# Kernel tuning notes

Hardware: AMD Instinct MI355X
Metric: run time of the kernel (lower is better)

The kernel has to match this reference:

```python
import jax, jax.numpy as jnp
import numpy as np

OUT, IN, GS = 16384, 4096, 16
G = OUT * IN // GS  # 4194304 groups


def setup_inputs() -> dict:
    key = jax.random.key(0)
    k1, k2, k3, k4 = jax.random.split(key, 4)
    x = jax.random.normal(k1, (8, 32, IN), dtype=jnp.float32)
    weight_q2 = jax.random.randint(k2, (G, GS // 4), 0, 256, dtype=jnp.int32)
    weight_norm = jax.random.uniform(k3, (G, 1), dtype=jnp.float16)
    bias = jax.random.normal(k4, (OUT,), dtype=jnp.float32)
    return {"x": x, "weight_q2": weight_q2, "weight_norm": weight_norm, "bias": bias}


def _dequant_2bit(weight_q2, weight_norm):
    # torch: xq_out[:, i::4] = (xq >> 2i) & 3  =>  element index within group = i + 4*k
    # where k = packed column (slow, stride 4), i = shift index (fast).
    norm = weight_norm.astype(jnp.float32)                      # [G, 1]
    shifts = jnp.arange(4, dtype=jnp.int32) * 2                 # [4]
    vals = (weight_q2[:, :, None] >> shifts) & 3                # [G, 4(pack k), 4(shift i)]
    xq_out = vals.astype(jnp.float32).reshape(G, GS)            # [G, 16], layout k*4 + i
    w = (xq_out / 3.0) * (2.0 * norm) - norm                    # [G, 16]
    return w.reshape(OUT, IN)


def reference(x, weight_q2, weight_norm, bias):
    w = _dequant_2bit(weight_q2, weight_norm)                   # [OUT, IN] fp32
    return jnp.einsum('bsi,oi->bso', x, w) + bias
```

## Files before the change

### kernel.cpp

```cpp
#include <hip/hip_runtime.h>
#include <stdint.h>

#define M_DIM 256
#define N_DIM 16384
#define K_DIM 4096
#define BN 32
#define BM 128
#define BK 128
#define NT2 (K_DIM / BK)

typedef __bf16 bf16x8 __attribute__((ext_vector_type(8)));
typedef float  f32x4  __attribute__((ext_vector_type(4)));

__device__ __forceinline__ uint32_t f2bf(float f) {
  uint32_t u = __float_as_uint(f);
  return (u + 0x7fffu + ((u >> 16) & 1u)) >> 16;
}

#define LDS_BARRIER() \
  asm volatile("s_waitcnt lgkmcnt(0)\n\ts_barrier" ::: "memory")

__global__ __launch_bounds__(256) void cvt_x_kernel(const float* __restrict__ x,
                                                    uint4* __restrict__ ws) {
  int T = blockIdx.x * 256 + threadIdx.x;
  int mb_glob = T >> 13;
  int r       = T & 8191;
  int kch     = r >> 6;
  int L       = r & 63;
  int row = mb_glob * 16 + (L & 15);
  int k   = kch * 32 + (L >> 4) * 8;
  const float* p = x + (size_t)row * K_DIM + k;
  float4 a = *(const float4*)p;
  float4 b = *(const float4*)(p + 4);
  uint4 o;
  o.x = f2bf(a.x) | (f2bf(a.y) << 16);
  o.y = f2bf(a.z) | (f2bf(a.w) << 16);
  o.z = f2bf(b.x) | (f2bf(b.y) << 16);
  o.w = f2bf(b.z) | (f2bf(b.w) << 16);
  ws[T] = o;
}

__device__ __forceinline__ uint4 deq8(uint2 q, float nv) {
  float a2 = nv * (2.0f / 3.0f);
  uint32_t tlo = f2bf(-nv) | (f2bf(fmaf(1.0f, a2, -nv)) << 16);
  uint32_t thi = f2bf(fmaf(2.0f, a2, -nv)) | (f2bf(fmaf(3.0f, a2, -nv)) << 16);
  uint32_t s0 = ((q.x & 3u) | ((q.x & 0xCu) << 14)) * 0x0202u + 0x01000100u;
  uint32_t s1 = (((q.x >> 4) & 3u) | ((q.x & 0xC0u) << 10)) * 0x0202u + 0x01000100u;
  uint32_t s2 = ((q.y & 3u) | ((q.y & 0xCu) << 14)) * 0x0202u + 0x01000100u;
  uint32_t s3 = (((q.y >> 4) & 3u) | ((q.y & 0xC0u) << 10)) * 0x0202u + 0x01000100u;
  uint4 r;
  r.x = __builtin_amdgcn_perm(thi, tlo, s0);
  r.y = __builtin_amdgcn_perm(thi, tlo, s1);
  r.z = __builtin_amdgcn_perm(thi, tlo, s2);
  r.w = __builtin_amdgcn_perm(thi, tlo, s3);
  return r;
}

__global__ __launch_bounds__(256, 4) void gemm2bit_kernel(
    const uint4*    __restrict__ aws,
    const uint32_t* __restrict__ q2,
    const float*    __restrict__ nrm,
    const float*    __restrict__ bias,
    float*          __restrict__ out)
{
  __shared__ uint4 Bb[2][512];

  const int tid  = threadIdx.x;
  const int lane = tid & 63;
  const int w    = tid >> 6;
  const int lo4  = lane & 15;
  const int qd   = lane >> 4;
  const int n0   = blockIdx.x * BN;
  const int m0   = blockIdx.y * BM;

  const int lrs = lane ^ qd;

  const int nloc = tid >> 3;
  const int kg   = (tid >> 1) & 3;
  const int h    = tid & 1;
  const int grow = n0 + nloc;
  const int qd2  = (kg & 1) * 2 + h;
  const int swz  = (nloc & 15) ^ qd2;
  const int bs0 = ((kg >> 1) * 2 + (nloc >> 4)) * 64 + qd2 * 16 + swz;
  const int bs1 = ((2 + (kg >> 1)) * 2 + (nloc >> 4)) * 64 + qd2 * 16 + swz;

  const uint4* pA = aws + (size_t)(blockIdx.y * 8 + w * 2) * 8192 + lane;
  const uint32_t* pq = q2 + ((size_t)grow * 256 + kg) * 4 + h * 2;
  const float*    pn = nrm + (size_t)grow * 256 + kg;

  f32x4 acc[2][2];
#pragma unroll
  for (int s = 0; s < 2; ++s)
#pragma unroll
    for (int u = 0; u < 2; ++u)
      acc[s][u] = (f32x4){0.f, 0.f, 0.f, 0.f};

  uint4 af0[8], af1[8];
  uint2 qa0, qa1, qb0, qb1;
  float na0, na1, nb0, nb1;

#pragma unroll
  for (int s = 0; s < 2; ++s)
#pragma unroll
    for (int c = 0; c < 4; ++c)
      af0[s * 4 + c] = pA[s * 8192 + c * 64];
  {
    uint2 x0 = *(const uint2*)pq;
    uint2 x1 = *(const uint2*)(pq + 16);
    float y0 = pn[0], y1 = pn[4];
    qa0 = *(const uint2*)(pq + 32);  qa1 = *(const uint2*)(pq + 48);
    na0 = pn[8];  na1 = pn[12];
    qb0 = *(const uint2*)(pq + 64);  qb1 = *(const uint2*)(pq + 80);
    nb0 = pn[16]; nb1 = pn[20];
    Bb[0][bs0] = deq8(x0, y0);
    Bb[0][bs1] = deq8(x1, y1);
  }
  LDS_BARRIER();
  const uint4* pAp = pA + 256;

#define GEMM_BODY(T, PR, AFC, AFN, Q0, Q1, N0v, N1v)                            \
  do {                                                                          \
    if ((T) + 1 < NT2) {                                                        \
      _Pragma("unroll")                                                         \
      for (int s = 0; s < 2; ++s)                                               \
        _Pragma("unroll")                                                       \
        for (int c = 0; c < 4; ++c)                                             \
          AFN[s * 4 + c] = pAp[s * 8192 + c * 64];                              \
    }                                                                           \
    _Pragma("unroll")                                                           \
    for (int c = 0; c < 4; ++c) {                                               \
      bf16x8 bfv[2];                                                            \
      _Pragma("unroll")                                                         \
      for (int u = 0; u < 2; ++u)                                               \
        bfv[u] = *(const bf16x8*)&Bb[PR][(c * 2 + u) * 64 + lrs];               \
      _Pragma("unroll")                                                         \
      for (int s = 0; s < 2; ++s) {                                             \
        bf16x8 av = __builtin_bit_cast(bf16x8, AFC[s * 4 + c]);                 \
        _Pragma("unroll")                                                       \
        for (int u = 0; u < 2; ++u)                                             \
          acc[s][u] = __builtin_amdgcn_mfma_f32_16x16x32_bf16(av, bfv[u],       \
                                                              acc[s][u], 0, 0, 0);\
      }                                                                         \
    }                                                                           \
    if ((T) + 1 < NT2) {                                                        \
      Bb[(PR) ^ 1][bs0] = deq8(Q0, N0v);                                        \
      Bb[(PR) ^ 1][bs1] = deq8(Q1, N1v);                                        \
    }                                                                           \
    if ((T) + 3 < NT2) {                                                        \
      Q0  = *(const uint2*)(pq + (size_t)((T) + 3) * 32);                       \
      Q1  = *(const uint2*)(pq + (size_t)((T) + 3) * 32 + 16);                  \
      N0v = pn[(size_t)((T) + 3) * 8];                                          \
      N1v = pn[(size_t)((T) + 3) * 8 + 4];                                      \
    }                                                                           \
    pAp += 256;                                                                 \
    LDS_BARRIER();                                                              \
  } while (0)

  for (int t2 = 0; t2 < NT2; t2 += 2) {
    GEMM_BODY(t2,     0, af0, af1, qa0, qa1, na0, na1);
    GEMM_BODY(t2 + 1, 1, af1, af0, qb0, qb1, nb0, nb1);
  }
#undef GEMM_BODY

  float bv[2];
#pragma unroll
  for (int u = 0; u < 2; ++u)
    bv[u] = bias[n0 + u * 16 + lo4];

#pragma unroll
  for (int s = 0; s < 2; ++s) {
    int mrow = m0 + w * 32 + s * 16 + qd * 4;
#pragma unroll
    for (int u = 0; u < 2; ++u) {
      int ncol = n0 + u * 16 + lo4;
      float* p = out + (size_t)mrow * N_DIM + ncol;
#pragma unroll
      for (int r = 0; r < 4; ++r)
        p[(size_t)r * N_DIM] = acc[s][u][r] + bv[u];
    }
  }
}

extern "C" void kernel_launch(void* const* d_in, const int* in_sizes, int n_in,
                              void* d_out, int out_size, void* d_ws, size_t ws_size,
                              hipStream_t stream) {
  const float*    x    = (const float*)d_in[0];
  const uint32_t* q2   = (const uint32_t*)d_in[1];
  const float*    nm   = (const float*)d_in[2];
  const float*    bias = (const float*)d_in[3];
  float*          out  = (float*)d_out;
  uint4*          aws  = (uint4*)d_ws;

  cvt_x_kernel<<<512, 256, 0, stream>>>(x, aws);
  gemm2bit_kernel<<<dim3(N_DIM / BN, 2), 256, 0, stream>>>(aws, q2, nm, bias, out);
}
```

Baseline: 176.1 us.

## Widen N tile to 64 with 512-thread blocks and 2x4 warp grid

Doubles the per-block N tile to 64 columns and uses 8 waves arranged as 4 (M) by 2 (N), so each block dequantizes 64 weight rows into a larger LDS buffer and each A fragment load serves twice the N columns. The dequant store is split between two halves of the MFMA loop, and s_setprio is raised around the MFMA sections so matrix work interleaves with the dequant and load work. The aim is to halve redundant loads of the converted activations per weight tile and improve latency hiding. In exchange, the grid has half as many blocks, each block is larger, and register and LDS pressure per block go up.

```diff
diff --git a/kernel.cpp b/kernel.cpp
--- a/kernel.cpp
+++ b/kernel.cpp
@@ -4,8 +4,7 @@
 #define M_DIM 256
 #define N_DIM 16384
 #define K_DIM 4096
-#define BN 32
-#define BM 128
+#define BN 64
 #define BK 128
 #define NT2 (K_DIM / BK)
 
@@ -56,22 +55,24 @@
   return r;
 }
 
-__global__ __launch_bounds__(256, 4) void gemm2bit_kernel(
+__global__ __launch_bounds__(512, 4) void gemm2bit_kernel(
     const uint4*    __restrict__ aws,
     const uint32_t* __restrict__ q2,
     const float*    __restrict__ nrm,
     const float*    __restrict__ bias,
     float*          __restrict__ out)
 {
-  __shared__ uint4 Bb[2][512];
+  __shared__ uint4 Bb[2][1024];
 
   const int tid  = threadIdx.x;
   const int lane = tid & 63;
   const int w    = tid >> 6;
+  const int wm   = w >> 1;
+  const int wn   = w & 1;
   const int lo4  = lane & 15;
   const int qd   = lane >> 4;
   const int n0   = blockIdx.x * BN;
-  const int m0   = blockIdx.y * BM;
+  const int m0   = blockIdx.y * 128;
 
   const int lrs = lane ^ qd;
 
@@ -80,11 +81,10 @@
   const int h    = tid & 1;
   const int grow = n0 + nloc;
   const int qd2  = (kg & 1) * 2 + h;
-  const int swz  = (nloc & 15) ^ qd2;
-  const int bs0 = ((kg >> 1) * 2 + (nloc >> 4)) * 64 + qd2 * 16 + swz;
-  const int bs1 = ((2 + (kg >> 1)) * 2 + (nloc >> 4)) * 64 + qd2 * 16 + swz;
-
-  const uint4* pA = aws + (size_t)(blockIdx.y * 8 + w * 2) * 8192 + lane;
+  const int bs1 = ((kg >> 1) * 4 + (nloc >> 4)) * 64 + qd2 * 16 +
+                  ((nloc & 15) ^ qd2);
+
+  const uint4* pA = aws + (size_t)(blockIdx.y * 8 + wm * 2) * 8192 + lane;
   const uint32_t* pq = q2 + ((size_t)grow * 256 + kg) * 4 + h * 2;
   const float*    pn = nrm + (size_t)grow * 256 + kg;
 
@@ -96,83 +96,95 @@
       acc[s][u] = (f32x4){0.f, 0.f, 0.f, 0.f};
 
   uint4 af0[8], af1[8];
-  uint2 qa0, qa1, qb0, qb1;
-  float na0, na1, nb0, nb1;
+  uint2 qE1, qE2, qO1, qO2;
+  float nE1, nE2, nO1, nO2;
 
 #pragma unroll
   for (int s = 0; s < 2; ++s)
 #pragma unroll
     for (int c = 0; c < 4; ++c)
-      af0[s * 4 + c] = pA[s * 8192 + c * 64];
+      af0[s * 4 + c] = pA[(size_t)s * 8192 + c * 64];
   {
-    uint2 x0 = *(const uint2*)pq;
-    uint2 x1 = *(const uint2*)(pq + 16);
-    float y0 = pn[0], y1 = pn[4];
-    qa0 = *(const uint2*)(pq + 32);  qa1 = *(const uint2*)(pq + 48);
-    na0 = pn[8];  na1 = pn[12];
-    qb0 = *(const uint2*)(pq + 64);  qb1 = *(const uint2*)(pq + 80);
-    nb0 = pn[16]; nb1 = pn[20];
-    Bb[0][bs0] = deq8(x0, y0);
-    Bb[0][bs1] = deq8(x1, y1);
+    uint2 x1 = *(const uint2*)pq;
+    uint2 x2 = *(const uint2*)(pq + 16);
+    float y1 = pn[0], y2 = pn[4];
+    qE1 = *(const uint2*)(pq + 32);  qE2 = *(const uint2*)(pq + 48);
+    nE1 = pn[8];   nE2 = pn[12];
+    qO1 = *(const uint2*)(pq + 64);  qO2 = *(const uint2*)(pq + 80);
+    nO1 = pn[16];  nO2 = pn[20];
+    Bb[0][bs1]       = deq8(x1, y1);
+    Bb[0][bs1 + 512] = deq8(x2, y2);
   }
   LDS_BARRIER();
-  const uint4* pAp = pA + 256;
-
-#define GEMM_BODY(T, PR, AFC, AFN, Q0, Q1, N0v, N1v)                            \
+
+  const uint4*    pAp = pA + 256;
+  const uint32_t* pqp = pq + 96;
+  const float*    pnp = pn + 24;
+
+#define MFMA_C2(PR, AFC, cbase)                                                 \
+  do {                                                                          \
+    __builtin_amdgcn_s_setprio(1);                                              \
+    _Pragma("unroll")                                                           \
+    for (int c = (cbase); c < (cbase) + 2; ++c) {                               \
+      bf16x8 bv0 = *(const bf16x8*)&Bb[PR][(c * 4 + wn * 2) * 64 + lrs];        \
+      bf16x8 bv1 = *(const bf16x8*)&Bb[PR][(c * 4 + wn * 2 + 1) * 64 + lrs];    \
+      _Pragma("unroll")                                                         \
+      for (int s = 0; s < 2; ++s) {                                             \
+        bf16x8 av = __builtin_bit_cast(bf16x8, AFC[s * 4 + c]);                 \
+        acc[s][0] = __builtin_amdgcn_mfma_f32_16x16x32_bf16(av, bv0,            \
+                                                            acc[s][0], 0, 0, 0);\
+        acc[s][1] = __builtin_amdgcn_mfma_f32_16x16x32_bf16(av, bv1,            \
+                                                            acc[s][1], 0, 0, 0);\
+      }                                                                         \
+    }                                                                           \
+    __builtin_amdgcn_s_setprio(0);                                              \
+  } while (0)
+
+#define GEMM_BODY(T, PR, AFC, AFN, Q1, Q2, N1v, N2v)                            \
   do {                                                                          \
     if ((T) + 1 < NT2) {                                                        \
       _Pragma("unroll")                                                         \
       for (int s = 0; s < 2; ++s)                                               \
         _Pragma("unroll")                                                       \
         for (int c = 0; c < 4; ++c)                                             \
-          AFN[s * 4 + c] = pAp[s * 8192 + c * 64];                              \
-    }                                                                           \
-    _Pragma("unroll")                                                           \
-    for (int c = 0; c < 4; ++c) {                                               \
-      bf16x8 bfv[2];                                                            \
-      _Pragma("unroll")                                                         \
-      for (int u = 0; u < 2; ++u)                                               \
-        bfv[u] = *(const bf16x8*)&Bb[PR][(c * 2 + u) * 64 + lrs];               \
-      _Pragma("unroll")                                                         \
-      for (int s = 0; s < 2; ++s) {                                             \
-        bf16x8 av = __builtin_bit_cast(bf16x8, AFC[s * 4 + c]);                 \
-        _Pragma("unroll")                                                       \
-        for (int u = 0; u < 2; ++u)                                             \
-          acc[s][u] = __builtin_amdgcn_mfma_f32_16x16x32_bf16(av, bfv[u],       \
-                                                              acc[s][u], 0, 0, 0);\
-      }                                                                         \
-    }                                                                           \
+          AFN[s * 4 + c] = pAp[(size_t)s * 8192 + c * 64];                      \
+    }                                                                           \
+    pAp += 256;                                                                 \
+    MFMA_C2(PR, AFC, 0);                                                        \
     if ((T) + 1 < NT2) {                                                        \
-      Bb[(PR) ^ 1][bs0] = deq8(Q0, N0v);                                        \
-      Bb[(PR) ^ 1][bs1] = deq8(Q1, N1v);                                        \
-    }                                                                           \
+      Bb[(PR) ^ 1][bs1]       = deq8(Q1, N1v);                                  \
+      Bb[(PR) ^ 1][bs1 + 512] = deq8(Q2, N2v);                                  \
+    }                                                                           \
+    MFMA_C2(PR, AFC, 2);                                                        \
     if ((T) + 3 < NT2) {                                                        \
-      Q0  = *(const uint2*)(pq + (size_t)((T) + 3) * 32);                       \
-      Q1  = *(const uint2*)(pq + (size_t)((T) + 3) * 32 + 16);                  \
-      N0v = pn[(size_t)((T) + 3) * 8];                                          \
-      N1v = pn[(size_t)((T) + 3) * 8 + 4];                                      \
-    }                                                                           \
-    pAp += 256;                                                                 \
+      Q1  = *(const uint2*)pqp;                                                 \
+      Q2  = *(const uint2*)(pqp + 16);                                          \
+      N1v = pnp[0];                                                             \
+      N2v = pnp[4];                                                             \
+    }                                                                           \
+    pqp += 32;                                                                  \
+    pnp += 8;                                                                   \
     LDS_BARRIER();                                                              \
   } while (0)
 
   for (int t2 = 0; t2 < NT2; t2 += 2) {
-    GEMM_BODY(t2,     0, af0, af1, qa0, qa1, na0, na1);
-    GEMM_BODY(t2 + 1, 1, af1, af0, qb0, qb1, nb0, nb1);
+    GEMM_BODY(t2,     0, af0, af1, qE1, qE2, nE1, nE2);
+    GEMM_BODY(t2 + 1, 1, af1, af0, qO1, qO2, nO1, nO2);
   }
 #undef GEMM_BODY
+#undef MFMA_C2
 
   float bv[2];
 #pragma unroll
   for (int u = 0; u < 2; ++u)
-    bv[u] = bias[n0 + u * 16 + lo4];
+    bv[u] = bias[n0 + wn * 32 + u * 16 + lo4];
 
 #pragma unroll
   for (int s = 0; s < 2; ++s) {
-    int mrow = m0 + w * 32 + s * 16 + qd * 4;
+    int mrow = m0 + wm * 32 + s * 16 + qd * 4;
 #pragma unroll
     for (int u = 0; u < 2; ++u) {
-      int ncol = n0 + u * 16 + lo4;
+      int ncol = n0 + wn * 32 + u * 16 + lo4;
       float* p = out + (size_t)mrow * N_DIM + ncol;
 #pragma unroll
       for (int r = 0; r < 4; ++r)
@@ -192,5 +204,5 @@
   uint4*          aws  = (uint4*)d_ws;
 
   cvt_x_kernel<<<512, 256, 0, stream>>>(x, aws);
-  gemm2bit_kernel<<<dim3(N_DIM / BN, 2), 256, 0, stream>>>(aws, q2, nm, bias, out);
-}
+  gemm2bit_kernel<<<dim3(N_DIM / BN, 2), 512, 0, stream>>>(aws, q2, nm, bias, out);
+}
```

After: 170.0 us. 1.04x faster.
